# Optimization experiments

Hardware: AMD Instinct MI355X
Metric: run time of the kernel (lower is better)

Reference implementation:

```python
import jax, jax.numpy as jnp
import numpy as np

B, T, C, H = 4, 2048, 1024, 16
HS = C // H
DFF = 4 * C
EPS = 1e-5


def setup_inputs() -> dict:
    key = jax.random.key(0)
    ks = jax.random.split(key, 8)
    s = 0.02
    inp = {
        "x": jax.random.normal(ks[0], (B, T, C), jnp.float32),
        # attention linear weights, stored (in, out) so h @ W + b
        "Wq": jax.random.normal(ks[1], (C, C), jnp.float32) * s,
        "bq": jnp.zeros((C,), jnp.float32),
        "Wk": jax.random.normal(ks[2], (C, C), jnp.float32) * s,
        "bk": jnp.zeros((C,), jnp.float32),
        "Wv": jax.random.normal(ks[3], (C, C), jnp.float32) * s,
        "bv": jnp.zeros((C,), jnp.float32),
        "Wo": jax.random.normal(ks[4], (C, C), jnp.float32) * s,
        "bo": jnp.zeros((C,), jnp.float32),
        # feed-forward
        "W1": jax.random.normal(ks[5], (C, DFF), jnp.float32) * s,
        "b1": jnp.zeros((DFF,), jnp.float32),
        "W2": jax.random.normal(ks[6], (DFF, C), jnp.float32) * s,
        "b2": jnp.zeros((C,), jnp.float32),
        # layernorms
        "g1": jnp.ones((C,), jnp.float32),
        "be1": jnp.zeros((C,), jnp.float32),
        "g2": jnp.ones((C,), jnp.float32),
        "be2": jnp.zeros((C,), jnp.float32),
    }
    return inp


def _layernorm(x, g, b):
    mu = jnp.mean(x, axis=-1, keepdims=True)
    var = jnp.mean(jnp.square(x - mu), axis=-1, keepdims=True)
    return (x - mu) * jax.lax.rsqrt(var + EPS) * g + b


def _attention(h, Wq, bq, Wk, bk, Wv, bv, Wo, bo):
    Bx, Tx, Cx = h.shape
    q = (h @ Wq + bq).reshape(Bx, Tx, H, HS).transpose(0, 2, 1, 3)  # [B,H,T,hs]
    k = (h @ Wk + bk).reshape(Bx, Tx, H, HS).transpose(0, 2, 1, 3)
    v = (h @ Wv + bv).reshape(Bx, Tx, H, HS).transpose(0, 2, 1, 3)
    att = jnp.einsum("bhqd,bhkd->bhqk", q, k) * (1.0 / np.sqrt(HS))
    causal = jnp.tril(jnp.ones((Tx, Tx), bool))
    att = jnp.where(causal, att, jnp.float32(-jnp.inf))
    att = jax.nn.softmax(att, axis=-1)
    y = jnp.einsum("bhqk,bhkd->bhqd", att, v)
    y = y.transpose(0, 2, 1, 3).reshape(Bx, Tx, Cx)
    return y @ Wo + bo


def reference(x, Wq, bq, Wk, bk, Wv, bv, Wo, bo, W1, b1, W2, b2, g1, be1, g2, be2):
    x = x + _attention(_layernorm(x, g1, be1), Wq, bq, Wk, bk, Wv, bv, Wo, bo)
    h = _layernorm(x, g2, be2)
    ff = jax.nn.relu(h @ W1 + b1) @ W2 + b2
    return x + ff
```

## Files before the change

### kernel.cpp

```cpp
#include <hip/hip_runtime.h>
#include <hip/hip_bf16.h>

#define Bq   4
#define Tq   2048
#define Cq   1024
#define Hq   16
#define HSq  64
#define DFFq 4096
#define Mq   (Bq*Tq)

typedef float f32x4  __attribute__((ext_vector_type(4)));
typedef short bf16x8 __attribute__((ext_vector_type(8)));

__device__ __forceinline__ float b2f(unsigned short u){ return __uint_as_float(((unsigned)u)<<16); }
__device__ __forceinline__ unsigned short f2b(float f){
  union { __hip_bfloat16 h; unsigned short u; } cv;
  cv.h = __float2bfloat16(f);
  return cv.u;
}
__device__ __forceinline__ unsigned pkbf(float a, float b){
  const unsigned ua = __float_as_uint(a) + 0x8000u;
  const unsigned ub = __float_as_uint(b) + 0x8000u;
  return (ua>>16) | (ub & 0xffff0000u);
}

__device__ __forceinline__ void gld_lds16(const unsigned short* g, unsigned short* l){
  __builtin_amdgcn_global_load_lds(
      (const __attribute__((address_space(1))) void*)g,
      (__attribute__((address_space(3))) void*)l, 16, 0, 0);
}

__device__ __forceinline__ int probe_bf16(const unsigned short* w){
  const int lane = threadIdx.x & 63;
  ushort4 u = *(const ushort4*)(w + lane*4);
  int cnt = 0;
  {
    unsigned e;
    e=(u.x>>7)&0xFF; cnt += (e>=0x60 && e<=0x7E);
    e=(u.y>>7)&0xFF; cnt += (e>=0x60 && e<=0x7E);
    e=(u.z>>7)&0xFF; cnt += (e>=0x60 && e<=0x7E);
    e=(u.w>>7)&0xFF; cnt += (e>=0x60 && e<=0x7E);
  }
#pragma unroll
  for (int off=1; off<64; off<<=1) cnt += __shfl_xor(cnt, off, 64);
  return cnt >= 224;
}

__global__ __launch_bounds__(256) void cvtvec_k(
    const void* s0,const void* s1,const void* s2,const void* s3,const void* s4,
    const void* s5,const void* s6,const void* s7,const void* s8,const void* s9,
    const unsigned short* __restrict__ probew, unsigned short* __restrict__ dst)
{
  const int isbf = probe_bf16(probew);
  const int idx = blockIdx.x*256 + threadIdx.x;
  const int seg = idx>>12, off = idx&4095;
  const void* s; int len;
  switch(seg){
    case 0: s=s0; len=1024; break;
    case 1: s=s1; len=1024; break;
    case 2: s=s2; len=1024; break;
    case 3: s=s3; len=1024; break;
    case 4: s=s4; len=4096; break;
    case 5: s=s5; len=1024; break;
    case 6: s=s6; len=1024; break;
    case 7: s=s7; len=1024; break;
    case 8: s=s8; len=1024; break;
    default: s=s9; len=1024; break;
  }
  if (off >= len) return;
  const float v = isbf ? b2f(((const unsigned short*)s)[off]) : ((const float*)s)[off];
  dst[idx] = f2b(v);
}

__global__ __launch_bounds__(256) void ln_k(const void* __restrict__ xin,
    const unsigned short* __restrict__ g, const unsigned short* __restrict__ be,
    unsigned short* __restrict__ out, const unsigned short* __restrict__ probew)
{
  const int isbf = probe_bf16(probew);
  const int row = blockIdx.x;
  const int tid = threadIdx.x;
  float v[4];
  if (isbf){
    const unsigned short* xr = (const unsigned short*)xin + (size_t)row*Cq;
    ushort4 u = *(const ushort4*)(xr + tid*4);
    v[0]=b2f(u.x); v[1]=b2f(u.y); v[2]=b2f(u.z); v[3]=b2f(u.w);
  } else {
    const float* xr = (const float*)xin + (size_t)row*Cq;
    float4 u = *(const float4*)(xr + tid*4);
    v[0]=u.x; v[1]=u.y; v[2]=u.z; v[3]=u.w;
  }
  float s  = v[0]+v[1]+v[2]+v[3];
  float ss = v[0]*v[0]+v[1]*v[1]+v[2]*v[2]+v[3]*v[3];
#pragma unroll
  for (int off=32; off>0; off>>=1){
    s  += __shfl_down(s,  off, 64);
    ss += __shfl_down(ss, off, 64);
  }
  __shared__ float sa[4], sb[4];
  const int wave = tid>>6, lane = tid&63;
  if (lane==0){ sa[wave]=s; sb[wave]=ss; }
  __syncthreads();
  s  = sa[0]+sa[1]+sa[2]+sa[3];
  ss = sb[0]+sb[1]+sb[2]+sb[3];
  const float mu  = s  * (1.0f/Cq);
  const float var = ss * (1.0f/Cq) - mu*mu;
  const float rs  = rsqrtf(fmaxf(var, 0.0f) + 1e-5f);
  ushort4 o; unsigned short* op = (unsigned short*)&o;
#pragma unroll
  for (int i=0;i<4;i++){
    const int ci = tid*4+i;
    op[i] = f2b((v[i]-mu)*rs*b2f(g[ci]) + b2f(be[ci]));
  }
  *(ushort4*)(out + (size_t)row*Cq + tid*4) = o;
}

__global__ __launch_bounds__(256) void wtrans4_k(
    const void* __restrict__ w0, const void* __restrict__ w1,
    const void* __restrict__ w2, const void* __restrict__ w3,
    unsigned short* __restrict__ Wqkv, unsigned short* __restrict__ WoT,
    const unsigned short* __restrict__ probew)
{
  const int isbf = probe_bf16(probew);
  const int z = blockIdx.z;
  const void* Win = (z==0)?w0 : (z==1)?w1 : (z==2)?w2 : w3;
  unsigned short* Wt = (z<3) ? (Wqkv + (size_t)z*1048576) : WoT;
  __shared__ __align__(16) unsigned short tile[64][72];
  const int kb = blockIdx.x, nb = blockIdx.y, tid = threadIdx.x;
#pragma unroll
  for (int i=0;i<2;i++){
    const int v = tid + i*256;
    const int kr = v>>3, nc = (v&7)*8;
    if (isbf){
      *(uint4*)&tile[kr][nc] =
        *(const uint4*)((const unsigned short*)Win + (size_t)(kb*64+kr)*1024 + nb*64 + nc);
    } else {
      const float* wp = (const float*)Win + (size_t)(kb*64+kr)*1024 + nb*64 + nc;
      float4 a = *(const float4*)wp, b = *(const float4*)(wp+4);
      alignas(16) unsigned short t[8] =
        {f2b(a.x),f2b(a.y),f2b(a.z),f2b(a.w),f2b(b.x),f2b(b.y),f2b(b.z),f2b(b.w)};
      *(uint4*)&tile[kr][nc] = *(const uint4*)t;
    }
  }
  __syncthreads();
#pragma unroll
  for (int i=0;i<2;i++){
    const int v = tid + i*256;
    const int nr = v>>3, kc = (v&7)*8;
    alignas(16) unsigned short tmp[8];
#pragma unroll
    for (int j=0;j<8;j++) tmp[j] = tile[kc+j][nr];
    *(uint4*)(Wt + (size_t)(nb*64+nr)*1024 + kb*64 + kc) = *(const uint4*)tmp;
  }
}

__global__ __launch_bounds__(256) void wtrans_k(const void* __restrict__ Win,
    unsigned short* __restrict__ Wt, const int Kd, const int Nd,
    const unsigned short* __restrict__ probew)
{
  const int isbf = probe_bf16(probew);
  __shared__ __align__(16) unsigned short tile[64][72];
  const int kb = blockIdx.x, nb = blockIdx.y, tid = threadIdx.x;
#pragma unroll
  for (int i=0;i<2;i++){
    const int v = tid + i*256;
    const int kr = v>>3, nc = (v&7)*8;
    if (isbf){
      *(uint4*)&tile[kr][nc] =
        *(const uint4*)((const unsigned short*)Win + (size_t)(kb*64+kr)*Nd + nb*64 + nc);
    } else {
      const float* wp = (const float*)Win + (size_t)(kb*64+kr)*Nd + nb*64 + nc;
      float4 a = *(const float4*)wp, b = *(const float4*)(wp+4);
      alignas(16) unsigned short t[8] =
        {f2b(a.x),f2b(a.y),f2b(a.z),f2b(a.w),f2b(b.x),f2b(b.y),f2b(b.z),f2b(b.w)};
      *(uint4*)&tile[kr][nc] = *(const uint4*)t;
    }
  }
  __syncthreads();
#pragma unroll
  for (int i=0;i<2;i++){
    const int v = tid + i*256;
    const int nr = v>>3, kc = (v&7)*8;
    alignas(16) unsigned short tmp[8];
#pragma unroll
    for (int j=0;j<8;j++) tmp[j] = tile[kc+j][nr];
    *(uint4*)(Wt + (size_t)(nb*64+nr)*Kd + kb*64 + kc) = *(const uint4*)tmp;
  }
}

template<int RELU, int RESMODE, int OUTMODE>
__global__ __launch_bounds__(512,2) void gemm256(
    const unsigned short* __restrict__ A,
    const unsigned short* __restrict__ Bt,
    const unsigned short* __restrict__ bias,
    const void* resid, void* outp,
    const int N, const int K, const int lda, const int ldb,
    const unsigned short* __restrict__ probew)
{
  int isbf = 1;
  if constexpr (OUTMODE==1 || OUTMODE==5 || RESMODE==2) isbf = probe_bf16(probew);

  int koff = 0;
  int nT = K >> 6;
  if constexpr (OUTMODE==5){
    if (isbf){
      if (blockIdx.z) return;
      nT = K >> 5;
    } else {
      koff = blockIdx.z * K;
    }
  }

  __shared__ __align__(16) unsigned short Al[3][256][64];
  __shared__ __align__(16) unsigned short Bl[3][128][64];

  const int tid  = threadIdx.x;
  const int lane = tid & 63, wave = tid >> 6;
  const int qd   = lane >> 4, c = lane & 15;
  const int m0   = blockIdx.x * 256, n0 = blockIdx.y * 128;
  const int wm   = (wave & 3) * 64;
  const int wn   = (wave >> 2) * 64;
  const int srow = tid >> 3;
  const int pg   = tid & 7;

  auto STAGE = [&](int t, int slot){
    const int k0 = koff + t*64;
#pragma unroll
    for (int i=0;i<4;i++){
      const int row = i*64 + srow;
      const int lg  = (pg + row) & 7;
      gld_lds16(A  + (size_t)(m0+row)*lda + k0 + lg*8, &Al[slot][row][pg*8]);
    }
#pragma unroll
    for (int i=0;i<2;i++){
      const int row = i*64 + srow;
      const int lg  = (pg + row) & 7;
      gld_lds16(Bt + (size_t)(n0+row)*ldb + k0 + lg*8, &Bl[slot][row][pg*8]);
    }
  };

  const f32x4 zf = {0.f,0.f,0.f,0.f};
  f32x4 acc[4][4];
#pragma unroll
  for (int i=0;i<4;i++)
#pragma unroll
    for (int j=0;j<4;j++) acc[i][j] = zf;

  STAGE(0,0);
  if (nT > 1) STAGE(1,1);

  const int rg0 = ((qd     - c) & 7) * 8;
  const int rg1 = ((4 + qd - c) & 7) * 8;

  int s = 0;
  for (int T=0; T<nT; ++T){
    if (T+1 < nT) { asm volatile("s_waitcnt vmcnt(6)" ::: "memory"); }
    else          { asm volatile("s_waitcnt vmcnt(0)" ::: "memory"); }
    __builtin_amdgcn_s_barrier();
    asm volatile("" ::: "memory");

    const unsigned short (*As)[64] = Al[s];
    const unsigned short (*Bs)[64] = Bl[s];

    bf16x8 af0[4], bf0[4];
#pragma unroll
    for (int mt=0;mt<4;mt++) af0[mt] = *(const bf16x8*)&As[wm+mt*16+c][rg0];
#pragma unroll
    for (int nt=0;nt<4;nt++) bf0[nt] = *(const bf16x8*)&Bs[wn+nt*16+c][rg0];

    if (T+2 < nT){
      const int ss = (s==0) ? 2 : s-1;
      STAGE(T+2, ss);
    }

    __builtin_amdgcn_s_setprio(1);
#pragma unroll
    for (int mt=0;mt<4;mt++)
#pragma unroll
      for (int nt=0;nt<4;nt++)
        acc[mt][nt] = __builtin_amdgcn_mfma_f32_16x16x32_bf16(af0[mt], bf0[nt], acc[mt][nt], 0,0,0);
    __builtin_amdgcn_s_setprio(0);

    bf16x8 af1[4], bf1[4];
#pragma unroll
    for (int mt=0;mt<4;mt++) af1[mt] = *(const bf16x8*)&As[wm+mt*16+c][rg1];
#pragma unroll
    for (int nt=0;nt<4;nt++) bf1[nt] = *(const bf16x8*)&Bs[wn+nt*16+c][rg1];

    __builtin_amdgcn_s_setprio(1);
#pragma unroll
    for (int mt=0;mt<4;mt++)
#pragma unroll
      for (int nt=0;nt<4;nt++)
        acc[mt][nt] = __builtin_amdgcn_mfma_f32_16x16x32_bf16(af1[mt], bf1[nt], acc[mt][nt], 0,0,0);
    __builtin_amdgcn_s_setprio(0);

    s = (s==2) ? 0 : s+1;
  }

  float bv[4];
  if constexpr (OUTMODE==3){
    const int segn = (n0+wn) >> 10;
    const unsigned short* bseg = bias + segn*4096;
#pragma unroll
    for (int nt=0;nt<4;nt++) bv[nt] = b2f(bseg[(n0+wn+nt*16+c)&1023]);
  } else {
#pragma unroll
    for (int nt=0;nt<4;nt++) bv[nt] = b2f(bias[n0+wn+nt*16+c]);
  }

#pragma unroll
  for (int mt=0;mt<4;mt++){
#pragma unroll
    for (int r=0;r<4;r++){
      const int m = m0 + wm + mt*16 + qd*4 + r;
#pragma unroll
      for (int nt=0;nt<4;nt++){
        const int n = n0 + wn + nt*16 + c;
        float val = acc[mt][nt][r] + ((OUTMODE==5 && !isbf && blockIdx.z!=0) ? 0.0f : bv[nt]);
        if (RELU) val = fmaxf(val, 0.0f);
        if constexpr (RESMODE==2){
          const size_t idx = (size_t)m*N + n;
          val += isbf ? b2f(((const unsigned short*)resid)[idx])
                      : ((const float*)resid)[idx];
        }
        if constexpr (OUTMODE==3){
          const int segn = (n0+wn) >> 10;
          const int n1 = n & 1023;
          unsigned short* dst = (unsigned short*)outp + (size_t)segn*8388608;
          if (segn < 2){
            dst[(size_t)m*1024 + n1] = f2b(val);
          } else {
            const size_t vidx = ((size_t)((m>>11)*16 + (n1>>6))*64 + (n1&63))*Tq + (m&2047);
            dst[vidx] = f2b(val);
          }
        } else if constexpr (OUTMODE==5){
          const size_t idx = (size_t)m*N + n;
          if (!isbf){
            atomicAdd((float*)outp + idx, val);
          } else {
            unsigned short* o16 = (unsigned short*)outp;
            o16[idx] = f2b(val + b2f(o16[idx]));
          }
        } else if constexpr (OUTMODE==1){
          const size_t idx = (size_t)m*N + n;
          if (isbf) ((unsigned short*)outp)[idx] = f2b(val);
          else      ((float*)outp)[idx] = val;
        } else {
          ((unsigned short*)outp)[(size_t)m*N + n] = f2b(val);
        }
      }
    }
  }
}

__global__ __launch_bounds__(256,3) void attn_k(const unsigned short* __restrict__ Qg,
    const unsigned short* __restrict__ Kg, const unsigned short* __restrict__ Vt,
    unsigned short* __restrict__ Y)
{
  const int bh = blockIdx.x;
  const int jq = (int)(gridDim.y - 1) - blockIdx.y;
  const int b = bh >> 4, h = bh & 15;
  const int tid = threadIdx.x, lane = tid & 63, wave = tid >> 6;
  const int qd = lane >> 4, c = lane & 15;
  const int q0  = jq * 128;
  const int wq0 = q0 + wave * 32;
  __shared__ __align__(16) unsigned short Kl[64*64];
  __shared__ __align__(16) unsigned short Vl[64*64];
  __shared__ __align__(16) unsigned short Pl[4][32][72];

  bf16x8 qf[2][2];
#pragma unroll
  for (int nt=0; nt<2; ++nt)
#pragma unroll
    for (int h2=0; h2<2; ++h2)
      qf[nt][h2] = *(const bf16x8*)(Qg + ((size_t)b*Tq + wq0 + nt*16 + c)*Cq
                                       + h*HSq + h2*32 + qd*8);

  const f32x4 zf = {0.f,0.f,0.f,0.f};
  const float NEG = -1.0e30f;
  f32x4 o[2][4];
  float lacc[2] = {0.f, 0.f};
#pragma unroll
  for (int nt=0;nt<2;nt++)
#pragma unroll
    for (int dt=0;dt<4;dt++) o[nt][dt]=zf;
  const float SCL = 0.125f * 1.44269504088896340736f;

  const int stg_r  = (lane>>3);
  const int stg_pg = lane & 7;

  const int r_row = (wave*2)*8 + stg_r;
  const unsigned short* kp0 = Kg + ((size_t)b*Tq + r_row)*Cq + h*HSq + ((stg_pg + r_row)&7)*8;
  const unsigned short* kp1 = Kg + ((size_t)b*Tq + r_row+8)*Cq + h*HSq + ((stg_pg + r_row+8)&7)*8;
  const unsigned short* vp0 = Vt + ((size_t)bh*HSq + r_row)*Tq + ((stg_pg + r_row)&7)*8;
  const unsigned short* vp1 = Vt + ((size_t)bh*HSq + r_row+8)*Tq + ((stg_pg + r_row+8)&7)*8;
  unsigned short* kl0 = &Kl[(r_row  )*64 + stg_pg*8];
  unsigned short* kl1 = &Kl[(r_row+8)*64 + stg_pg*8];
  unsigned short* vl0 = &Vl[(r_row  )*64 + stg_pg*8];
  unsigned short* vl1 = &Vl[(r_row+8)*64 + stg_pg*8];

  const int nkt = 2*(jq+1);
  for (int kt=0; kt<nkt; ++kt){
    const int k0 = kt*64;
    gld_lds16(kp0, kl0);  gld_lds16(kp1, kl1);
    gld_lds16(vp0, vl0);  gld_lds16(vp1, vl1);
    kp0 += 64*Cq; kp1 += 64*Cq; vp0 += 64; vp1 += 64;
    __syncthreads();

    if (k0 <= wq0 + 31){
      bf16x8 kf[4][2], vf[4][2];
#pragma unroll
      for (int mt=0;mt<4;mt++)
#pragma unroll
        for (int h2=0;h2<2;h2++){
          kf[mt][h2] = *(const bf16x8*)&Kl[(mt*16+c)*64 + ((h2*4+qd-c)&7)*8];
          vf[mt][h2] = *(const bf16x8*)&Vl[(mt*16+c)*64 + ((h2*4+qd-c)&7)*8];
        }
      const int domask = (k0 + 63 > wq0) ? 1 : 0;
#pragma unroll
      for (int nt=0; nt<2; ++nt){
        const int query = wq0 + nt*16 + c;
        f32x4 s[4];
#pragma unroll
        for (int mt=0;mt<4;mt++){
          f32x4 sa = zf;
          sa = __builtin_amdgcn_mfma_f32_16x16x32_bf16(kf[mt][0], qf[nt][0], sa, 0,0,0);
          sa = __builtin_amdgcn_mfma_f32_16x16x32_bf16(kf[mt][1], qf[nt][1], sa, 0,0,0);
          s[mt] = sa;
        }
        float p[4][4];
        float rs = 0.f;
#pragma unroll
        for (int mt=0;mt<4;mt++)
#pragma unroll
          for (int r=0;r<4;r++){
            float xv = fminf(s[mt][r]*SCL, 80.0f);
            if (domask && (k0 + mt*16 + qd*4 + r > query)) xv = NEG;
            const float pe = exp2f(xv);
            p[mt][r] = pe;
            rs += pe;
          }
        lacc[nt] += rs;
#pragma unroll
        for (int mt=0;mt<4;mt++){
          uint2 w2v;
          w2v.x = pkbf(p[mt][0], p[mt][1]);
          w2v.y = pkbf(p[mt][2], p[mt][3]);
          *(uint2*)&Pl[wave][nt*16+c][mt*16+qd*4] = w2v;
        }
        bf16x8 pf0 = *(const bf16x8*)&Pl[wave][nt*16+c][qd*8];
        bf16x8 pf1 = *(const bf16x8*)&Pl[wave][nt*16+c][32+qd*8];
#pragma unroll
        for (int dt=0;dt<4;dt++){
          o[nt][dt] = __builtin_amdgcn_mfma_f32_16x16x32_bf16(vf[dt][0], pf0, o[nt][dt], 0,0,0);
          o[nt][dt] = __builtin_amdgcn_mfma_f32_16x16x32_bf16(vf[dt][1], pf1, o[nt][dt], 0,0,0);
        }
      }
    }
    __syncthreads();
  }

#pragma unroll
  for (int nt=0;nt<2;nt++){
    lacc[nt] += __shfl_xor(lacc[nt], 16, 64);
    lacc[nt] += __shfl_xor(lacc[nt], 32, 64);
  }
#pragma unroll
  for (int nt=0;nt<2;nt++){
    const float inv = 1.0f / lacc[nt];
#pragma unroll
    for (int dt=0;dt<4;dt++){
      uint2 w2v;
      w2v.x = pkbf(o[nt][dt][0]*inv, o[nt][dt][1]*inv);
      w2v.y = pkbf(o[nt][dt][2]*inv, o[nt][dt][3]*inv);
      *(uint2*)&Pl[wave][nt*16+c][dt*16+qd*4] = w2v;
    }
  }
#pragma unroll
  for (int pass=0; pass<4; ++pass){
    const int qrow = pass*8 + (lane>>3);
    const int dcol = (lane&7)*8;
    uint4 val = *(const uint4*)&Pl[wave][qrow][dcol];
    *(uint4*)(Y + ((size_t)b*Tq + wq0 + qrow)*Cq + h*HSq + dcol) = val;
  }
}

extern "C" void kernel_launch(void* const* d_in, const int* in_sizes, int n_in,
                              void* d_out, int out_size, void* d_ws, size_t ws_size,
                              hipStream_t stream)
{
  (void)in_sizes; (void)n_in; (void)out_size; (void)ws_size;
  const void* x   = d_in[0];
  const void* Wq  = d_in[1];
  const void* Wk  = d_in[3];
  const void* Wv  = d_in[5];
  const void* Wo  = d_in[7];
  const void* W1  = d_in[9];
  const void* W2  = d_in[11];
  const unsigned short* pw = (const unsigned short*)W1;

  char* ws = (char*)d_ws;
  const size_t MB = 1u<<20;
  unsigned short* W1T   = (unsigned short*)(ws + 0*MB);
  unsigned short* W2T   = (unsigned short*)(ws + 8*MB);
  unsigned short* WqkvT = (unsigned short*)(ws + 16*MB);
  unsigned short* WoT   = (unsigned short*)(ws + 22*MB);
  unsigned short* Qb    = (unsigned short*)(ws + 24*MB);
  unsigned short* Kb    = (unsigned short*)(ws + 40*MB);
  unsigned short* Vt    = (unsigned short*)(ws + 56*MB);
  unsigned short* ff1   = (unsigned short*)(ws + 16*MB);
  unsigned short* hy    = (unsigned short*)(ws + 80*MB);
  unsigned short* vec   = (unsigned short*)(ws + 96*MB);
  unsigned short* vbo = vec + 12288;
  unsigned short* vb1 = vec + 16384;  unsigned short* vb2 = vec + 20480;
  unsigned short* vg1 = vec + 24576;  unsigned short* vbe1= vec + 28672;
  unsigned short* vg2 = vec + 32768;  unsigned short* vbe2= vec + 36864;

  const dim3 blk(256,1,1);
  const dim3 blk512(512,1,1);

  cvtvec_k<<<dim3(160), blk, 0, stream>>>(d_in[2], d_in[4], d_in[6], d_in[8],
      d_in[10], d_in[12], d_in[13], d_in[14], d_in[15], d_in[16], pw, vec);

  wtrans4_k<<<dim3(16,16,4), blk, 0, stream>>>(Wq, Wk, Wv, Wo, WqkvT, WoT, pw);
  wtrans_k<<<dim3(16,64), blk, 0, stream>>>(W1, W1T, 1024, 4096, pw);
  wtrans_k<<<dim3(64,16), blk, 0, stream>>>(W2, W2T, 4096, 1024, pw);

  ln_k<<<dim3(Mq), blk, 0, stream>>>(x, vg1, vbe1, hy, pw);

  gemm256<0,0,3><<<dim3(32,24), blk512, 0, stream>>>(hy, WqkvT, vec, nullptr, Qb,
      3072, 1024, 1024, 1024, pw);

  attn_k<<<dim3(64,16), blk, 0, stream>>>(Qb, Kb, Vt, hy);

  gemm256<0,2,1><<<dim3(32,8), blk512, 0, stream>>>(hy, WoT, vbo, x, d_out,
      1024, 1024, 1024, 1024, pw);

  ln_k<<<dim3(Mq), blk, 0, stream>>>(d_out, vg2, vbe2, hy, pw);

  gemm256<1,0,0><<<dim3(32,32), blk512, 0, stream>>>(hy, W1T, vb1, nullptr, ff1,
      4096, 1024, 1024, 1024, pw);
  gemm256<0,0,5><<<dim3(32,8,2), blk512, 0, stream>>>(ff1, W2T, vb2, nullptr, d_out,
      1024, 2048, 4096, 4096, pw);
}
```

Measured before the change: 555.4 us.

## Split GEMM tile staging into halves interleaved with MFMA phases and extra barriers

Restructures the GEMM main loop: the global-to-LDS prefetch of tile T+2 is split into two half-groups, each issued right after the LDS fragment reads of one K-half, with barriers around each MFMA phase. The loop is peeled so the last two iterations skip staging and the wait-count handling is explicit. The aim is to spread memory issue more evenly across compute phases and smooth contention between LDS reads and async loads. It adds several extra workgroup barriers per K tile, which may cost more than the overlap gains.

Measured after the change: 542.3 us. 1.02x faster.

```diff
diff --git a/kernel.cpp b/kernel.cpp
--- a/kernel.cpp
+++ b/kernel.cpp
@@ -222,17 +222,17 @@
   const int srow = tid >> 3;
   const int pg   = tid & 7;
 
-  auto STAGE = [&](int t, int slot){
+  auto STAGEg = [&](int t, int slot, int g){
     const int k0 = koff + t*64;
-#pragma unroll
-    for (int i=0;i<4;i++){
-      const int row = i*64 + srow;
+    const int ib = g*2;
+#pragma unroll
+    for (int i=0;i<2;i++){
+      const int row = (ib+i)*64 + srow;
       const int lg  = (pg + row) & 7;
-      gld_lds16(A  + (size_t)(m0+row)*lda + k0 + lg*8, &Al[slot][row][pg*8]);
-    }
-#pragma unroll
-    for (int i=0;i<2;i++){
-      const int row = i*64 + srow;
+      gld_lds16(A + (size_t)(m0+row)*lda + k0 + lg*8, &Al[slot][row][pg*8]);
+    }
+    {
+      const int row = g*64 + srow;
       const int lg  = (pg + row) & 7;
       gld_lds16(Bt + (size_t)(n0+row)*ldb + k0 + lg*8, &Bl[slot][row][pg*8]);
     }
@@ -245,57 +245,62 @@
 #pragma unroll
     for (int j=0;j<4;j++) acc[i][j] = zf;
 
-  STAGE(0,0);
-  if (nT > 1) STAGE(1,1);
-
   const int rg0 = ((qd     - c) & 7) * 8;
   const int rg1 = ((4 + qd - c) & 7) * 8;
 
-  int s = 0;
-  for (int T=0; T<nT; ++T){
-    if (T+1 < nT) { asm volatile("s_waitcnt vmcnt(6)" ::: "memory"); }
-    else          { asm volatile("s_waitcnt vmcnt(0)" ::: "memory"); }
-    __builtin_amdgcn_s_barrier();
-    asm volatile("" ::: "memory");
-
+  STAGEg(0,0,0); STAGEg(0,0,1);
+  STAGEg(1,1,0); STAGEg(1,1,1);
+  asm volatile("s_waitcnt vmcnt(6)" ::: "memory");
+  __builtin_amdgcn_s_barrier();
+
+  auto ktile = [&](int T, int s, bool stg, int wmode){
     const unsigned short (*As)[64] = Al[s];
     const unsigned short (*Bs)[64] = Bl[s];
-
-    bf16x8 af0[4], bf0[4];
-#pragma unroll
-    for (int mt=0;mt<4;mt++) af0[mt] = *(const bf16x8*)&As[wm+mt*16+c][rg0];
-#pragma unroll
-    for (int nt=0;nt<4;nt++) bf0[nt] = *(const bf16x8*)&Bs[wn+nt*16+c][rg0];
-
-    if (T+2 < nT){
-      const int ss = (s==0) ? 2 : s-1;
-      STAGE(T+2, ss);
-    }
-
+    const int ss = (s >= 1) ? s-1 : 2;
+    bf16x8 af[4], bfr[4];
+
+#pragma unroll
+    for (int mt=0;mt<4;mt++) af[mt]  = *(const bf16x8*)&As[wm+mt*16+c][rg0];
+#pragma unroll
+    for (int nt=0;nt<4;nt++) bfr[nt] = *(const bf16x8*)&Bs[wn+nt*16+c][rg0];
+    if (stg) STAGEg(T+2, ss, 0);
+    __builtin_amdgcn_s_barrier();
     __builtin_amdgcn_s_setprio(1);
 #pragma unroll
     for (int mt=0;mt<4;mt++)
 #pragma unroll
       for (int nt=0;nt<4;nt++)
-        acc[mt][nt] = __builtin_amdgcn_mfma_f32_16x16x32_bf16(af0[mt], bf0[nt], acc[mt][nt], 0,0,0);
+        acc[mt][nt] = __builtin_amdgcn_mfma_f32_16x16x32_bf16(af[mt], bfr[nt], acc[mt][nt], 0,0,0);
     __builtin_amdgcn_s_setprio(0);
-
-    bf16x8 af1[4], bf1[4];
-#pragma unroll
-    for (int mt=0;mt<4;mt++) af1[mt] = *(const bf16x8*)&As[wm+mt*16+c][rg1];
-#pragma unroll
-    for (int nt=0;nt<4;nt++) bf1[nt] = *(const bf16x8*)&Bs[wn+nt*16+c][rg1];
-
+    __builtin_amdgcn_s_barrier();
+
+#pragma unroll
+    for (int mt=0;mt<4;mt++) af[mt]  = *(const bf16x8*)&As[wm+mt*16+c][rg1];
+#pragma unroll
+    for (int nt=0;nt<4;nt++) bfr[nt] = *(const bf16x8*)&Bs[wn+nt*16+c][rg1];
+    if (stg) STAGEg(T+2, ss, 1);
+    __builtin_amdgcn_s_barrier();
     __builtin_amdgcn_s_setprio(1);
 #pragma unroll
     for (int mt=0;mt<4;mt++)
 #pragma unroll
       for (int nt=0;nt<4;nt++)
-        acc[mt][nt] = __builtin_amdgcn_mfma_f32_16x16x32_bf16(af1[mt], bf1[nt], acc[mt][nt], 0,0,0);
+        acc[mt][nt] = __builtin_amdgcn_mfma_f32_16x16x32_bf16(af[mt], bfr[nt], acc[mt][nt], 0,0,0);
     __builtin_amdgcn_s_setprio(0);
 
+    if (wmode == 6)      asm volatile("s_waitcnt vmcnt(6)" ::: "memory");
+    else if (wmode == 0) asm volatile("s_waitcnt vmcnt(0)" ::: "memory");
+    if (wmode >= 0) __builtin_amdgcn_s_barrier();
+  };
+
+  int s = 0;
+  for (int T=0; T<nT-2; ++T){
+    ktile(T, s, true, 6);
     s = (s==2) ? 0 : s+1;
   }
+  ktile(nT-2, s, false, 0);
+  s = (s==2) ? 0 : s+1;
+  ktile(nT-1, s, false, -1);
 
   float bv[4];
   if constexpr (OUTMODE==3){
```
